# Optimization experiments

Measured on AMD Instinct MI355X. Metric: run time of the kernel, lower is better.

The kernel has to match this reference:

```python
import jax, jax.numpy as jnp
import numpy as np

EPS = 1e-8      # laplace_transform epsilon
RC = 0.5        # residual_coff
L = 2           # num_layers
NU, NB, NI, D = 100000, 30000, 50000, 128
E_UB, E_UI, E_BI = 300000, 500000, 500000


def _l2norm(x):
    # F.normalize(x, p=2, dim=1)
    n = jnp.linalg.norm(x, axis=1, keepdims=True)
    return x / jnp.maximum(n, 1e-12)


def _spmm(rows, cols, vals, feats, n):
    # sparse (COO) matmul: out[r] += vals[e] * feats[cols[e]]
    return jax.ops.segment_sum(vals[:, None] * feats[cols], rows, num_segments=n)


def _sym_norm_graph(u, v, na, nb):
    # bipartite block matrix [[0, B],[B^T, 0]] with D^-1/2 A D^-1/2 normalization
    rows = jnp.concatenate([u, v + na])
    cols = jnp.concatenate([v + na, u])
    deg = jax.ops.segment_sum(jnp.ones(rows.shape[0], jnp.float32), rows,
                              num_segments=na + nb)
    dinv = 1.0 / (jnp.sqrt(deg) + EPS)
    vals = dinv[rows] * dinv[cols]
    return rows, cols, vals


def _one_propagate(rows, cols, vals, afeat, bfeat):
    n = afeat.shape[0] + bfeat.shape[0]
    feats = jnp.concatenate([afeat, bfeat], axis=0)
    ini = _l2norm(feats)
    acc = feats  # all_feats starts with raw feats, summed at the end
    for i in range(L):
        feats = _spmm(rows, cols, vals, feats, n)
        feats = (feats + RC * ini) / (i + 2)
        feats = _l2norm(feats)
        acc = acc + feats
    return acc[:afeat.shape[0]], acc[afeat.shape[0]:]


def setup_inputs() -> dict:
    key = jax.random.key(0)
    ks = jax.random.split(key, 10)
    return {
        "users_feat": jax.random.normal(ks[0], (NU, D), jnp.float32) * 0.1,
        "bundles_feat": jax.random.normal(ks[1], (NB, D), jnp.float32) * 0.1,
        "items_feat": jax.random.normal(ks[2], (NI, D), jnp.float32) * 0.1,
        "bi_vals": jax.random.uniform(ks[3], (E_BI,), jnp.float32),
        "ub_u": jax.random.randint(ks[4], (E_UB,), 0, NU),
        "ub_b": jax.random.randint(ks[5], (E_UB,), 0, NB),
        "ui_u": jax.random.randint(ks[6], (E_UI,), 0, NU),
        "ui_i": jax.random.randint(ks[7], (E_UI,), 0, NI),
        "bi_b": jax.random.randint(ks[8], (E_BI,), 0, NB),
        "bi_i": jax.random.randint(ks[9], (E_BI,), 0, NI),
    }


def reference(users_feat, bundles_feat, items_feat, bi_vals,
              ub_u, ub_b, ui_u, ui_i, bi_b, bi_i):
    nu, nb, ni = users_feat.shape[0], bundles_feat.shape[0], items_feat.shape[0]
    # UB (history) propagation
    r, c, v = _sym_norm_graph(ub_u, ub_b, nu, nb)
    hist_users, hist_bundles = _one_propagate(r, c, v, users_feat, bundles_feat)
    # UI (affinity) propagation
    r, c, v = _sym_norm_graph(ui_u, ui_i, nu, ni)
    aff_users, ui_items = _one_propagate(r, c, v, users_feat, items_feat)
    # BI aggregation: bundles x items sparse graph @ item features
    aff_bundles = _spmm(bi_b, bi_i, bi_vals, ui_items, nb)
    # concat [aff_users, hist_users, aff_bundles, hist_bundles] along rows
    return jnp.concatenate([aff_users, hist_users, aff_bundles, hist_bundles], axis=0)
```

## Files before the change

### kernel.cpp

```cpp
#include <hip/hip_runtime.h>

#define FD   128
#define FDH  64
#define EPSN 1e-8f
#define RCC  0.5f
#define SCAN_TPB 256
#define SCAN_ELEMS 1024

typedef unsigned int uint;
typedef unsigned short u16;
typedef unsigned char u8;
typedef float fx2 __attribute__((ext_vector_type(2)));

__device__ __forceinline__ float wave_sum(float x) {
#pragma unroll
    for (int off = 32; off > 0; off >>= 1) x += __shfl_xor(x, off);
    return x;
}

__device__ __forceinline__ uint packbf2(float a, float b) {
    uint ua = __float_as_uint(a); ua += 0x7fffu + ((ua >> 16) & 1u);
    uint ub = __float_as_uint(b); ub += 0x7fffu + ((ub >> 16) & 1u);
    return (ua >> 16) | (ub & 0xffff0000u);
}
__device__ __forceinline__ float2 unpackbf2(uint v) {
    return make_float2(__uint_as_float(v << 16), __uint_as_float(v & 0xffff0000u));
}
__device__ __forceinline__ u16 packfp8(float a, float b) {
    return (u16)__builtin_amdgcn_cvt_pk_fp8_f32(a, b, 0, false);
}

__global__ void passA(const int* __restrict__ ub_u, const int* __restrict__ ub_b,
                      const int* __restrict__ ui_u, const int* __restrict__ ui_i,
                      const int* __restrict__ bi_b, const int* __restrict__ bi_i,
                      const float* __restrict__ uf, const float* __restrict__ bf,
                      const float* __restrict__ itf,
                      int E_UB, int E_UI, int E_BI, int NU, int NB, int n1, int n2, int NT,
                      int nblk_edges,
                      int* __restrict__ head, int2* __restrict__ pairLL,
                      uint* __restrict__ fini16, float* __restrict__ normf) {
    if ((int)blockIdx.x < nblk_edges) {
        int e = blockIdx.x * blockDim.x + threadIdx.x;
        if (e < E_UB) {
            int a = ub_u[e], b = ub_b[e] + NU;
            int s0 = 2 * e;
            int p0 = atomicExch(&head[a], s0);
            int p1 = atomicExch(&head[b], s0 + 1);
            ((int4*)pairLL)[e] = make_int4(p0, b, p1, a);
        } else if (e < E_UB + E_UI) {
            int f = e - E_UB;
            int a = ui_u[f], bl = ui_i[f] + NU;
            int s0 = 2 * E_UB + 2 * f;
            int p0 = atomicExch(&head[n1 + a], s0);
            int p1 = atomicExch(&head[n1 + bl], s0 + 1);
            ((int4*)pairLL)[E_UB + f] = make_int4(p0, bl, p1, a);
        } else if (e < E_UB + E_UI + E_BI) {
            int g = e - E_UB - E_UI;
            int s = 2 * E_UB + 2 * E_UI + g;
            int p = atomicExch(&head[n1 + n2 + bi_b[g]], s);
            pairLL[s] = make_int2(p, bi_i[g]);
        }
    } else {
        int w = (((int)blockIdx.x - nblk_edges) * blockDim.x + threadIdx.x) >> 6;
        int lane = threadIdx.x & 63;
        if (w >= NT) return;
        const float* src = (w < NU) ? uf + (size_t)w * FD
                         : (w < NU + NB) ? bf + (size_t)(w - NU) * FD
                         : itf + (size_t)(w - NU - NB) * FD;
        float2 x = ((const float2*)src)[lane];
        float ss = wave_sum(x.x * x.x + x.y * x.y);
        float nrm = sqrtf(ss);
        float inv = 1.0f / fmaxf(nrm, 1e-12f);
        fini16[(size_t)w * FDH + lane] = packbf2(x.x * inv, x.y * inv);
        if (lane == 0) normf[w] = nrm;
    }
}

__global__ void passB(const int* __restrict__ head, const int2* __restrict__ pairLL,
                      int NN, int n12, int* __restrict__ deg, float* __restrict__ dinv) {
    int r = blockIdx.x * blockDim.x + threadIdx.x;
    if (r > NN) return;
    if (r == NN) { deg[NN] = 0; return; }
    int c = 0;
    int s = head[r];
    while (s >= 0) { c++; s = pairLL[s].x; }
    deg[r] = c;
    if (r < n12) dinv[r] = 1.0f / (sqrtf((float)c) + EPSN);
}

__global__ void scan_a(const int* __restrict__ in, int* __restrict__ out,
                       int* __restrict__ bsum, int nelem) {
    __shared__ int tsum[SCAN_TPB];
    int tid = threadIdx.x;
    int base = blockIdx.x * SCAN_ELEMS + tid * 4;
    int v0 = (base + 0 < nelem) ? in[base + 0] : 0;
    int v1 = (base + 1 < nelem) ? in[base + 1] : 0;
    int v2 = (base + 2 < nelem) ? in[base + 2] : 0;
    int v3 = (base + 3 < nelem) ? in[base + 3] : 0;
    int s = v0 + v1 + v2 + v3;
    tsum[tid] = s;
    __syncthreads();
    for (int off = 1; off < SCAN_TPB; off <<= 1) {
        int y = (tid >= off) ? tsum[tid - off] : 0;
        __syncthreads();
        tsum[tid] += y;
        __syncthreads();
    }
    int excl = tsum[tid] - s;
    if (tid == SCAN_TPB - 1) bsum[blockIdx.x] = tsum[SCAN_TPB - 1];
    if (base + 0 < nelem) out[base + 0] = excl;
    excl += v0;
    if (base + 1 < nelem) out[base + 1] = excl;
    excl += v1;
    if (base + 2 < nelem) out[base + 2] = excl;
    excl += v2;
    if (base + 3 < nelem) out[base + 3] = excl;
}

__global__ void scan_b(int* __restrict__ bsum, int nb) {
    __shared__ int sm[512];
    int tid = threadIdx.x;
    int v = (tid < nb) ? bsum[tid] : 0;
    sm[tid] = v;
    __syncthreads();
    for (int off = 1; off < 512; off <<= 1) {
        int y = (tid >= off) ? sm[tid - off] : 0;
        __syncthreads();
        sm[tid] += y;
        __syncthreads();
    }
    if (tid < nb) bsum[tid] = sm[tid] - v;
}

__global__ void scan_c(int* __restrict__ out, const int* __restrict__ bsum, int nelem) {
    int base = blockIdx.x * SCAN_ELEMS + threadIdx.x * 4;
    int add = bsum[blockIdx.x];
#pragma unroll
    for (int k = 0; k < 4; ++k)
        if (base + k < nelem) out[base + k] += add;
}

__global__ void passC_conv(const int* __restrict__ head, const int2* __restrict__ pairLL,
                           const int* __restrict__ rowptr, const float* __restrict__ bi_vals,
                           int NN, int n12, int S1,
                           int* __restrict__ cols, int2* __restrict__ bi2,
                           const uint* __restrict__ fini16, const float* __restrict__ normf,
                           const float* __restrict__ dinv,
                           int n1, int NU, int NB, u16* __restrict__ g8, int nblkC) {
    if ((int)blockIdx.x < nblkC) {
        int r = blockIdx.x * blockDim.x + threadIdx.x;
        if (r >= NN) return;
        int pos = rowptr[r];
        int s = head[r];
        if (r < n12) {
            while (s >= 0) { int2 p = pairLL[s]; cols[pos++] = p.y << 7; s = p.x; }
        } else {
            while (s >= 0) {
                int2 p = pairLL[s];
                bi2[pos - S1] = make_int2(p.y << 8, __float_as_int(bi_vals[s - S1]));
                pos++; s = p.x;
            }
        }
    } else {
        int w = (((int)blockIdx.x - nblkC) * blockDim.x + threadIdx.x) >> 6;
        int lane = threadIdx.x & 63;
        if (w >= n12) return;
        int node = (w < n1) ? w : ((w - n1 < NU) ? (w - n1) : (w - n1 + NB));
        float sc = dinv[w] * normf[node];
        float2 f = unpackbf2(fini16[(size_t)node * FDH + lane]);
        g8[(size_t)w * FDH + lane] = packfp8(f.x * sc, f.y * sc);
    }
}

#define ACC8(XU)  {                                                              \
    fx2 _pa = __builtin_amdgcn_cvt_pk_f32_fp8((int)(XU).x, false);               \
    fx2 _pb = __builtin_amdgcn_cvt_pk_f32_fp8((int)(XU).x, true);                \
    fx2 _pc = __builtin_amdgcn_cvt_pk_f32_fp8((int)(XU).y, false);               \
    fx2 _pd = __builtin_amdgcn_cvt_pk_f32_fp8((int)(XU).y, true);                \
    a0 += _pa.x; a1 += _pa.y; a2 += _pb.x; a3 += _pb.y;                          \
    a4 += _pc.x; a5 += _pc.y; a6 += _pd.x; a7 += _pd.y; }

#define GATHER8(TAB)                                                             \
    float a0=0.f,a1=0.f,a2=0.f,a3=0.f,a4=0.f,a5=0.f,a6=0.f,a7=0.f;               \
    {                                                                            \
      int base = lane & 32;                                                      \
      for (int cs = s; cs < e; cs += 32) {                                       \
        int cnt = e - cs; if (cnt > 32) cnt = 32;                                \
        int colv = (l31 < cnt) ? cols[cs + l31] : 0;                             \
        int p = 0;                                                               \
        for (; 2 * p + 8 <= cnt; p += 4) {                                       \
            int o0 = __shfl(colv, base + 2 * p + sub);                           \
            int o1 = __shfl(colv, base + 2 * p + 2 + sub);                       \
            int o2 = __shfl(colv, base + 2 * p + 4 + sub);                       \
            int o3 = __shfl(colv, base + 2 * p + 6 + sub);                       \
            uint2 x0 = *(const uint2*)(TAB + o0);                                \
            uint2 x1 = *(const uint2*)(TAB + o1);                                \
            uint2 x2 = *(const uint2*)(TAB + o2);                                \
            uint2 x3 = *(const uint2*)(TAB + o3);                                \
            ACC8(x0) ACC8(x1) ACC8(x2) ACC8(x3)                                  \
        }                                                                        \
        for (; 2 * p + 2 <= cnt; ++p) {                                          \
            int o = __shfl(colv, base + 2 * p + sub);                            \
            uint2 x = *(const uint2*)(TAB + o);                                  \
            ACC8(x)                                                              \
        }                                                                        \
        if (2 * p < cnt) {                                                       \
            int o = __shfl(colv, base + 2 * p);                                  \
            if (sub == 0) { uint2 x = *(const uint2*)(TAB + o); ACC8(x) }        \
        }                                                                        \
      }                                                                          \
    }                                                                            \
    a0 += __shfl_xor(a0, 16); a1 += __shfl_xor(a1, 16);                          \
    a2 += __shfl_xor(a2, 16); a3 += __shfl_xor(a3, 16);                          \
    a4 += __shfl_xor(a4, 16); a5 += __shfl_xor(a5, 16);                          \
    a6 += __shfl_xor(a6, 16); a7 += __shfl_xor(a7, 16);

__global__ void spmm_L1(const int* __restrict__ rowptr, const int* __restrict__ cols,
                        const float* __restrict__ dinv, const float* __restrict__ normf,
                        const uint* __restrict__ fini16, const u16* __restrict__ g8,
                        uint* __restrict__ facc16, uint* __restrict__ fX8,
                        int n1, int NU, int NB, int n12) {
    int wv = (blockIdx.x * blockDim.x + threadIdx.x) >> 6;
    int lane = threadIdx.x & 63;
    int hw = lane >> 5, l31 = lane & 31, sub = (lane >> 4) & 1, t = lane & 15;
    int r = 2 * wv + hw;
    if (r >= n12) return;
    int s = rowptr[r], e = rowptr[r + 1];
    bool ui = (r >= n1);
    int node = ui ? ((r - n1 < NU) ? (r - n1) : (r - n1 + NB)) : r;
    float dr = dinv[r];
    uint4 iu = ((const uint4*)(fini16 + (size_t)node * FDH))[t];
    float nr = normf[node];
    const u8* tab = (const u8*)g8 + ((size_t)(ui ? n1 : 0) << 7) + (t << 3);
    GATHER8(tab)
    float2 i01 = unpackbf2(iu.x), i23 = unpackbf2(iu.y);
    float2 i45 = unpackbf2(iu.z), i67 = unpackbf2(iu.w);
    float v0 = (dr * a0 + RCC * i01.x) * 0.5f;
    float v1 = (dr * a1 + RCC * i01.y) * 0.5f;
    float v2 = (dr * a2 + RCC * i23.x) * 0.5f;
    float v3 = (dr * a3 + RCC * i23.y) * 0.5f;
    float v4 = (dr * a4 + RCC * i45.x) * 0.5f;
    float v5 = (dr * a5 + RCC * i45.y) * 0.5f;
    float v6 = (dr * a6 + RCC * i67.x) * 0.5f;
    float v7 = (dr * a7 + RCC * i67.y) * 0.5f;
    float sq = v0*v0 + v1*v1 + v2*v2 + v3*v3 + v4*v4 + v5*v5 + v6*v6 + v7*v7;
#pragma unroll
    for (int off = 8; off > 0; off >>= 1) sq += __shfl_xor(sq, off);
    float inv = 1.0f / fmaxf(sqrtf(sq), 1e-12f);
    v0 *= inv; v1 *= inv; v2 *= inv; v3 *= inv;
    v4 *= inv; v5 *= inv; v6 *= inv; v7 *= inv;
    if (sub == 0) {
        uint4 fa;
        fa.x = packbf2(fmaf(i01.x, nr, v0), fmaf(i01.y, nr, v1));
        fa.y = packbf2(fmaf(i23.x, nr, v2), fmaf(i23.y, nr, v3));
        fa.z = packbf2(fmaf(i45.x, nr, v4), fmaf(i45.y, nr, v5));
        fa.w = packbf2(fmaf(i67.x, nr, v6), fmaf(i67.y, nr, v7));
        ((uint4*)(facc16 + (size_t)r * FDH))[t] = fa;
        int xa = __builtin_amdgcn_cvt_pk_fp8_f32(v0 * dr, v1 * dr, 0, false);
        xa = __builtin_amdgcn_cvt_pk_fp8_f32(v2 * dr, v3 * dr, xa, true);
        int xb = __builtin_amdgcn_cvt_pk_fp8_f32(v4 * dr, v5 * dr, 0, false);
        xb = __builtin_amdgcn_cvt_pk_fp8_f32(v6 * dr, v7 * dr, xb, true);
        ((uint2*)(fX8 + (size_t)r * 32))[t] = make_uint2((uint)xa, (uint)xb);
    }
}

__global__ void spmm_L2(const int* __restrict__ rowptr, const int* __restrict__ cols,
                        const float* __restrict__ dinv, const uint* __restrict__ fini16,
                        const uint* __restrict__ facc16, const uint* __restrict__ fX8,
                        uint* __restrict__ items16, float* __restrict__ outp,
                        int n1, int NU, int NB, int n12) {
    int wv = (blockIdx.x * blockDim.x + threadIdx.x) >> 6;
    int lane = threadIdx.x & 63;
    int hw = lane >> 5, l31 = lane & 31, sub = (lane >> 4) & 1, t = lane & 15;
    int r = 2 * wv + hw;
    if (r >= n12) return;
    int s = rowptr[r], e = rowptr[r + 1];
    bool ui = (r >= n1);
    int node = ui ? ((r - n1 < NU) ? (r - n1) : (r - n1 + NB)) : r;
    float dr = dinv[r];
    uint4 iu = ((const uint4*)(fini16 + (size_t)node * FDH))[t];
    uint4 au = ((const uint4*)(facc16 + (size_t)r * FDH))[t];
    const u8* tab = (const u8*)fX8 + ((size_t)(ui ? n1 : 0) << 7) + (t << 3);
    GATHER8(tab)
    float2 i01 = unpackbf2(iu.x), i23 = unpackbf2(iu.y);
    float2 i45 = unpackbf2(iu.z), i67 = unpackbf2(iu.w);
    float v0 = (dr * a0 + RCC * i01.x) * (1.0f / 3.0f);
    float v1 = (dr * a1 + RCC * i01.y) * (1.0f / 3.0f);
    float v2 = (dr * a2 + RCC * i23.x) * (1.0f / 3.0f);
    float v3 = (dr * a3 + RCC * i23.y) * (1.0f / 3.0f);
    float v4 = (dr * a4 + RCC * i45.x) * (1.0f / 3.0f);
    float v5 = (dr * a5 + RCC * i45.y) * (1.0f / 3.0f);
    float v6 = (dr * a6 + RCC * i67.x) * (1.0f / 3.0f);
    float v7 = (dr * a7 + RCC * i67.y) * (1.0f / 3.0f);
    float sq = v0*v0 + v1*v1 + v2*v2 + v3*v3 + v4*v4 + v5*v5 + v6*v6 + v7*v7;
#pragma unroll
    for (int off = 8; off > 0; off >>= 1) sq += __shfl_xor(sq, off);
    float inv = 1.0f / fmaxf(sqrtf(sq), 1e-12f);
    v0 *= inv; v1 *= inv; v2 *= inv; v3 *= inv;
    v4 *= inv; v5 *= inv; v6 *= inv; v7 *= inv;
    float2 a01 = unpackbf2(au.x), a23 = unpackbf2(au.y);
    float2 a45 = unpackbf2(au.z), a67 = unpackbf2(au.w);
    float n0 = a01.x + v0, n1v = a01.y + v1, n2v = a23.x + v2, n3 = a23.y + v3;
    float n4 = a45.x + v4, n5 = a45.y + v5, n6 = a67.x + v6, n7 = a67.y + v7;
    if (sub == 0) {
        if (!ui) {
            size_t dst = (r < NU) ? (size_t)(NU + r) : (size_t)(2 * NU + NB + (r - NU));
            float* orow = outp + dst * FD;
            ((float4*)orow)[2 * t]     = make_float4(n0, n1v, n2v, n3);
            ((float4*)orow)[2 * t + 1] = make_float4(n4, n5, n6, n7);
        } else {
            int l = r - n1;
            if (l < NU) {
                float* orow = outp + (size_t)l * FD;
                ((float4*)orow)[2 * t]     = make_float4(n0, n1v, n2v, n3);
                ((float4*)orow)[2 * t + 1] = make_float4(n4, n5, n6, n7);
            } else {
                uint4 it;
                it.x = packbf2(n0, n1v);
                it.y = packbf2(n2v, n3);
                it.z = packbf2(n4, n5);
                it.w = packbf2(n6, n7);
                ((uint4*)(items16 + (size_t)(l - NU) * FDH))[t] = it;
            }
        }
    }
}

#define FMA8(XU, W) { float2 _f;                                                 \
    _f = unpackbf2((XU).x); a0 = fmaf(W, _f.x, a0); a1 = fmaf(W, _f.y, a1);      \
    _f = unpackbf2((XU).y); a2 = fmaf(W, _f.x, a2); a3 = fmaf(W, _f.y, a3);      \
    _f = unpackbf2((XU).z); a4 = fmaf(W, _f.x, a4); a5 = fmaf(W, _f.y, a5);      \
    _f = unpackbf2((XU).w); a6 = fmaf(W, _f.x, a6); a7 = fmaf(W, _f.y, a7); }

__global__ void bi_gather(const int* __restrict__ rowptr, const int2* __restrict__ bi2,
                          int S1, const uint* __restrict__ items16,
                          float* __restrict__ outb, int nb) {
    int wv = (blockIdx.x * blockDim.x + threadIdx.x) >> 6;
    int lane = threadIdx.x & 63;
    int hw = lane >> 5, l31 = lane & 31, sub = (lane >> 4) & 1, t = lane & 15;
    int r = 2 * wv + hw;
    if (r >= nb) return;
    int s = rowptr[r], e = rowptr[r + 1];
    const u8* tab = (const u8*)items16 + (t << 4);
    float a0=0.f,a1=0.f,a2=0.f,a3=0.f,a4=0.f,a5=0.f,a6=0.f,a7=0.f;
    int base = lane & 32;
    for (int cs = s; cs < e; cs += 32) {
        int cnt = e - cs; if (cnt > 32) cnt = 32;
        int2 cv = (l31 < cnt) ? bi2[cs + l31 - S1] : make_int2(0, 0);
        int p = 0;
        for (; 2 * p + 8 <= cnt; p += 4) {
            int o0 = __shfl(cv.x, base + 2 * p + sub);
            int o1 = __shfl(cv.x, base + 2 * p + 2 + sub);
            int o2 = __shfl(cv.x, base + 2 * p + 4 + sub);
            int o3 = __shfl(cv.x, base + 2 * p + 6 + sub);
            float w0 = __int_as_float(__shfl(cv.y, base + 2 * p + sub));
            float w1 = __int_as_float(__shfl(cv.y, base + 2 * p + 2 + sub));
            float w2 = __int_as_float(__shfl(cv.y, base + 2 * p + 4 + sub));
            float w3 = __int_as_float(__shfl(cv.y, base + 2 * p + 6 + sub));
            uint4 x0 = *(const uint4*)(tab + o0);
            uint4 x1 = *(const uint4*)(tab + o1);
            uint4 x2 = *(const uint4*)(tab + o2);
            uint4 x3 = *(const uint4*)(tab + o3);
            FMA8(x0, w0) FMA8(x1, w1) FMA8(x2, w2) FMA8(x3, w3)
        }
        for (; 2 * p + 2 <= cnt; ++p) {
            int o = __shfl(cv.x, base + 2 * p + sub);
            float wt = __int_as_float(__shfl(cv.y, base + 2 * p + sub));
            uint4 x = *(const uint4*)(tab + o);
            FMA8(x, wt)
        }
        if (2 * p < cnt) {
            int o = __shfl(cv.x, base + 2 * p);
            float wt = __int_as_float(__shfl(cv.y, base + 2 * p));
            if (sub == 0) { uint4 x = *(const uint4*)(tab + o); FMA8(x, wt) }
        }
    }
    a0 += __shfl_xor(a0, 16); a1 += __shfl_xor(a1, 16);
    a2 += __shfl_xor(a2, 16); a3 += __shfl_xor(a3, 16);
    a4 += __shfl_xor(a4, 16); a5 += __shfl_xor(a5, 16);
    a6 += __shfl_xor(a6, 16); a7 += __shfl_xor(a7, 16);
    if (sub == 0) {
        float* orow = outb + (size_t)r * FD;
        ((float4*)orow)[2 * t]     = make_float4(a0, a1, a2, a3);
        ((float4*)orow)[2 * t + 1] = make_float4(a4, a5, a6, a7);
    }
}

extern "C" void kernel_launch(void* const* d_in, const int* in_sizes, int n_in,
                              void* d_out, int out_size, void* d_ws, size_t ws_size,
                              hipStream_t stream) {
    const float* users   = (const float*)d_in[0];
    const float* bundles = (const float*)d_in[1];
    const float* items   = (const float*)d_in[2];
    const float* bi_vals = (const float*)d_in[3];
    const int* ub_u = (const int*)d_in[4];
    const int* ub_b = (const int*)d_in[5];
    const int* ui_u = (const int*)d_in[6];
    const int* ui_i = (const int*)d_in[7];
    const int* bi_b = (const int*)d_in[8];
    const int* bi_i = (const int*)d_in[9];

    const int NU = in_sizes[0] / FD;
    const int NB = in_sizes[1] / FD;
    const int NI = in_sizes[2] / FD;
    const int E_BI = in_sizes[3];
    const int E_UB = in_sizes[4];
    const int E_UI = in_sizes[6];
    float* out = (float*)d_out;

    const int n1 = NU + NB, n2 = NU + NI;
    const int n12 = n1 + n2;
    const int NT = NU + NB + NI;
    const int NN = n12 + NB;
    const int S1 = 2 * E_UB + 2 * E_UI;
    const int TOT = S1 + E_BI;
    const int ETOT = E_UB + E_UI + E_BI;

    uint* fini16   = (uint*)d_ws;
    uint* facc16   = fini16 + (size_t)NT * FDH;
    uint* items16  = facc16 + (size_t)n12 * FDH;
    u16* g8        = (u16*)(items16 + (size_t)NI * FDH);
    uint* fX8      = (uint*)(g8 + (size_t)n12 * FDH);
    float* normf   = (float*)(fX8 + (size_t)n12 * 32);
    float* dinv    = normf + NT;
    int* deg       = (int*)(dinv + n12);
    int* rowptr    = deg + (NN + 1);
    int* head      = rowptr + (NN + 1);
    int* bsum      = head + NN;
    int* cols      = bsum + 512;
    int2* bi2      = (int2*)((((size_t)(cols + S1)) + 15) & ~(size_t)15);
    int2* pairLL   = (int2*)((((size_t)(bi2 + E_BI)) + 15) & ~(size_t)15);

    dim3 blk(256);
    auto rows_grid  = [](int n) { return dim3((unsigned)((n + 3) / 4)); };
    auto rows2_grid = [](int n) { return dim3((unsigned)((n + 7) / 8)); };
    auto thr_grid   = [](int n) { return dim3((unsigned)((n + 255) / 256)); };

    hipMemsetAsync(head, 0xFF, (size_t)NN * 4, stream);
    int nblk_edges = (ETOT + 255) / 256;
    int nblk_prep  = (NT + 3) / 4;
    passA<<<dim3((unsigned)(nblk_edges + nblk_prep)), blk, 0, stream>>>(
        ub_u, ub_b, ui_u, ui_i, bi_b, bi_i, users, bundles, items,
        E_UB, E_UI, E_BI, NU, NB, n1, n2, NT, nblk_edges,
        head, pairLL, fini16, normf);
    passB<<<thr_grid(NN + 1), blk, 0, stream>>>(head, pairLL, NN, n12, deg, dinv);
    {
        int nelem = NN + 1;
        int nblk = (nelem + SCAN_ELEMS - 1) / SCAN_ELEMS;
        scan_a<<<dim3((unsigned)nblk), dim3(SCAN_TPB), 0, stream>>>(deg, rowptr, bsum, nelem);
        scan_b<<<dim3(1), dim3(512), 0, stream>>>(bsum, nblk);
        scan_c<<<dim3((unsigned)nblk), dim3(SCAN_TPB), 0, stream>>>(rowptr, bsum, nelem);
    }
    {
        int nblkC = (NN + 255) / 256;
        int nblkG = (n12 + 3) / 4;
        passC_conv<<<dim3((unsigned)(nblkC + nblkG)), blk, 0, stream>>>(
            head, pairLL, rowptr, bi_vals, NN, n12, S1, cols, bi2,
            fini16, normf, dinv, n1, NU, NB, g8, nblkC);
    }

    spmm_L1<<<rows2_grid(n12), blk, 0, stream>>>(rowptr, cols, dinv, normf,
                                                 fini16, g8, facc16, fX8, n1, NU, NB, n12);
    spmm_L2<<<rows2_grid(n12), blk, 0, stream>>>(rowptr, cols, dinv, fini16,
                                                 facc16, fX8, items16, out, n1, NU, NB, n12);
    bi_gather<<<rows2_grid(NB), blk, 0, stream>>>(rowptr + n12, bi2, S1, items16,
        out + (size_t)2 * NU * FD, NB);
}
```

Measured before the change: 601.8 us.

## Quantize layer-1 propagated features to FP4 with per-row scale for layer-2 gather

```diff
diff --git a/kernel.cpp b/kernel.cpp
--- a/kernel.cpp
+++ b/kernel.cpp
@@ -11,6 +11,18 @@
 typedef unsigned short u16;
 typedef unsigned char u8;
 typedef float fx2 __attribute__((ext_vector_type(2)));
+typedef int iv4 __attribute__((ext_vector_type(4)));
+typedef int iv2 __attribute__((ext_vector_type(2)));
+
+#if __has_builtin(__builtin_amdgcn_cvt_scalef32_pk_f32_fp4) && __has_builtin(__builtin_amdgcn_cvt_scalef32_pk_fp4_f32)
+#define USE_FP4 1
+#define COLSHIFT 6
+#define L1SHIFT 1
+#else
+#define USE_FP4 0
+#define COLSHIFT 7
+#define L1SHIFT 0
+#endif
 
 __device__ __forceinline__ float wave_sum(float x) {
 #pragma unroll
@@ -46,19 +58,22 @@
             int s0 = 2 * e;
             int p0 = atomicExch(&head[a], s0);
             int p1 = atomicExch(&head[b], s0 + 1);
-            ((int4*)pairLL)[e] = make_int4(p0, b, p1, a);
+            iv4 rec = {p0, b, p1, a};
+            __builtin_nontemporal_store(rec, (iv4*)pairLL + e);
         } else if (e < E_UB + E_UI) {
             int f = e - E_UB;
             int a = ui_u[f], bl = ui_i[f] + NU;
             int s0 = 2 * E_UB + 2 * f;
             int p0 = atomicExch(&head[n1 + a], s0);
             int p1 = atomicExch(&head[n1 + bl], s0 + 1);
-            ((int4*)pairLL)[E_UB + f] = make_int4(p0, bl, p1, a);
+            iv4 rec = {p0, bl, p1, a};
+            __builtin_nontemporal_store(rec, (iv4*)pairLL + (E_UB + f));
         } else if (e < E_UB + E_UI + E_BI) {
             int g = e - E_UB - E_UI;
             int s = 2 * E_UB + 2 * E_UI + g;
             int p = atomicExch(&head[n1 + n2 + bi_b[g]], s);
-            pairLL[s] = make_int2(p, bi_i[g]);
+            iv2 rec = {p, bi_i[g]};
+            __builtin_nontemporal_store(rec, (iv2*)pairLL + s);
         }
     } else {
         int w = (((int)blockIdx.x - nblk_edges) * blockDim.x + threadIdx.x) >> 6;
@@ -71,7 +86,8 @@
         float ss = wave_sum(x.x * x.x + x.y * x.y);
         float nrm = sqrtf(ss);
         float inv = 1.0f / fmaxf(nrm, 1e-12f);
-        fini16[(size_t)w * FDH + lane] = packbf2(x.x * inv, x.y * inv);
+        __builtin_nontemporal_store(packbf2(x.x * inv, x.y * inv),
+                                    &fini16[(size_t)w * FDH + lane]);
         if (lane == 0) normf[w] = nrm;
     }
 }
@@ -153,7 +169,7 @@
         int pos = rowptr[r];
         int s = head[r];
         if (r < n12) {
-            while (s >= 0) { int2 p = pairLL[s]; cols[pos++] = p.y << 7; s = p.x; }
+            while (s >= 0) { int2 p = pairLL[s]; cols[pos++] = p.y << COLSHIFT; s = p.x; }
         } else {
             while (s >= 0) {
                 int2 p = pairLL[s];
@@ -180,7 +196,7 @@
     a0 += _pa.x; a1 += _pa.y; a2 += _pb.x; a3 += _pb.y;                          \
     a4 += _pc.x; a5 += _pc.y; a6 += _pd.x; a7 += _pd.y; }
 
-#define GATHER8(TAB)                                                             \
+#define GATHER8(TAB, SH)                                                         \
     float a0=0.f,a1=0.f,a2=0.f,a3=0.f,a4=0.f,a5=0.f,a6=0.f,a7=0.f;               \
     {                                                                            \
       int base = lane & 32;                                                      \
@@ -189,10 +205,10 @@
         int colv = (l31 < cnt) ? cols[cs + l31] : 0;                             \
         int p = 0;                                                               \
         for (; 2 * p + 8 <= cnt; p += 4) {                                       \
-            int o0 = __shfl(colv, base + 2 * p + sub);                           \
-            int o1 = __shfl(colv, base + 2 * p + 2 + sub);                       \
-            int o2 = __shfl(colv, base + 2 * p + 4 + sub);                       \
-            int o3 = __shfl(colv, base + 2 * p + 6 + sub);                       \
+            int o0 = __shfl(colv, base + 2 * p + sub) << (SH);                   \
+            int o1 = __shfl(colv, base + 2 * p + 2 + sub) << (SH);               \
+            int o2 = __shfl(colv, base + 2 * p + 4 + sub) << (SH);               \
+            int o3 = __shfl(colv, base + 2 * p + 6 + sub) << (SH);               \
             uint2 x0 = *(const uint2*)(TAB + o0);                                \
             uint2 x1 = *(const uint2*)(TAB + o1);                                \
             uint2 x2 = *(const uint2*)(TAB + o2);                                \
@@ -200,12 +216,12 @@
             ACC8(x0) ACC8(x1) ACC8(x2) ACC8(x3)                                  \
         }                                                                        \
         for (; 2 * p + 2 <= cnt; ++p) {                                          \
-            int o = __shfl(colv, base + 2 * p + sub);                            \
+            int o = __shfl(colv, base + 2 * p + sub) << (SH);                    \
             uint2 x = *(const uint2*)(TAB + o);                                  \
             ACC8(x)                                                              \
         }                                                                        \
         if (2 * p < cnt) {                                                       \
-            int o = __shfl(colv, base + 2 * p);                                  \
+            int o = __shfl(colv, base + 2 * p) << (SH);                          \
             if (sub == 0) { uint2 x = *(const uint2*)(TAB + o); ACC8(x) }        \
         }                                                                        \
       }                                                                          \
@@ -215,10 +231,66 @@
     a4 += __shfl_xor(a4, 16); a5 += __shfl_xor(a5, 16);                          \
     a6 += __shfl_xor(a6, 16); a7 += __shfl_xor(a7, 16);
 
+#if USE_FP4
+#define ACC4(XU, SV)  {                                                          \
+    fx2 _f;                                                                      \
+    _f = __builtin_amdgcn_cvt_scalef32_pk_f32_fp4((XU), 1.0f, 0);                \
+    a0 = fmaf(SV, _f.x, a0); a1 = fmaf(SV, _f.y, a1);                            \
+    _f = __builtin_amdgcn_cvt_scalef32_pk_f32_fp4((XU), 1.0f, 1);                \
+    a2 = fmaf(SV, _f.x, a2); a3 = fmaf(SV, _f.y, a3);                            \
+    _f = __builtin_amdgcn_cvt_scalef32_pk_f32_fp4((XU), 1.0f, 2);                \
+    a4 = fmaf(SV, _f.x, a4); a5 = fmaf(SV, _f.y, a5);                            \
+    _f = __builtin_amdgcn_cvt_scalef32_pk_f32_fp4((XU), 1.0f, 3);                \
+    a6 = fmaf(SV, _f.x, a6); a7 = fmaf(SV, _f.y, a7); }
+
+#define GATHER4(TAB, FSC)                                                        \
+    float a0=0.f,a1=0.f,a2=0.f,a3=0.f,a4=0.f,a5=0.f,a6=0.f,a7=0.f;               \
+    {                                                                            \
+      int base = lane & 32;                                                      \
+      for (int cs = s; cs < e; cs += 32) {                                       \
+        int cnt = e - cs; if (cnt > 32) cnt = 32;                                \
+        int colv = (l31 < cnt) ? cols[cs + l31] : 0;                             \
+        float sclv = (FSC)[colv >> 6];                                           \
+        int p = 0;                                                               \
+        for (; 2 * p + 8 <= cnt; p += 4) {                                       \
+            int o0 = __shfl(colv, base + 2 * p + sub);                           \
+            int o1 = __shfl(colv, base + 2 * p + 2 + sub);                       \
+            int o2 = __shfl(colv, base + 2 * p + 4 + sub);                       \
+            int o3 = __shfl(colv, base + 2 * p + 6 + sub);                       \
+            float s0v = __shfl(sclv, base + 2 * p + sub);                        \
+            float s1v = __shfl(sclv, base + 2 * p + 2 + sub);                    \
+            float s2v = __shfl(sclv, base + 2 * p + 4 + sub);                    \
+            float s3v = __shfl(sclv, base + 2 * p + 6 + sub);                    \
+            uint x0 = *(const uint*)(TAB + o0);                                  \
+            uint x1 = *(const uint*)(TAB + o1);                                  \
+            uint x2 = *(const uint*)(TAB + o2);                                  \
+            uint x3 = *(const uint*)(TAB + o3);                                  \
+            ACC4(x0, s0v) ACC4(x1, s1v) ACC4(x2, s2v) ACC4(x3, s3v)              \
+        }                                                                        \
+        for (; 2 * p + 2 <= cnt; ++p) {                                          \
+            int o = __shfl(colv, base + 2 * p + sub);                            \
+            float sv = __shfl(sclv, base + 2 * p + sub);                         \
+            uint x = *(const uint*)(TAB + o);                                    \
+            ACC4(x, sv)                                                          \
+        }                                                                        \
+        if (2 * p < cnt) {                                                       \
+            int o = __shfl(colv, base + 2 * p);                                  \
+            float sv = __shfl(sclv, base + 2 * p);                               \
+            if (sub == 0) { uint x = *(const uint*)(TAB + o); ACC4(x, sv) }      \
+        }                                                                        \
+      }                                                                          \
+    }                                                                            \
+    a0 += __shfl_xor(a0, 16); a1 += __shfl_xor(a1, 16);                          \
+    a2 += __shfl_xor(a2, 16); a3 += __shfl_xor(a3, 16);                          \
+    a4 += __shfl_xor(a4, 16); a5 += __shfl_xor(a5, 16);                          \
+    a6 += __shfl_xor(a6, 16); a7 += __shfl_xor(a7, 16);
+#endif
+
 __global__ void spmm_L1(const int* __restrict__ rowptr, const int* __restrict__ cols,
                         const float* __restrict__ dinv, const float* __restrict__ normf,
                         const uint* __restrict__ fini16, const u16* __restrict__ g8,
-                        uint* __restrict__ facc16, uint* __restrict__ fX8,
+                        uint* __restrict__ facc16, uint* __restrict__ fX,
+                        float* __restrict__ fscale,
                         int n1, int NU, int NB, int n12) {
     int wv = (blockIdx.x * blockDim.x + threadIdx.x) >> 6;
     int lane = threadIdx.x & 63;
@@ -232,7 +304,7 @@
     uint4 iu = ((const uint4*)(fini16 + (size_t)node * FDH))[t];
     float nr = normf[node];
     const u8* tab = (const u8*)g8 + ((size_t)(ui ? n1 : 0) << 7) + (t << 3);
-    GATHER8(tab)
+    GATHER8(tab, L1SHIFT)
     float2 i01 = unpackbf2(iu.x), i23 = unpackbf2(iu.y);
     float2 i45 = unpackbf2(iu.z), i67 = unpackbf2(iu.w);
     float v0 = (dr * a0 + RCC * i01.x) * 0.5f;
@@ -256,17 +328,37 @@
         fa.z = packbf2(fmaf(i45.x, nr, v4), fmaf(i45.y, nr, v5));
         fa.w = packbf2(fmaf(i67.x, nr, v6), fmaf(i67.y, nr, v7));
         ((uint4*)(facc16 + (size_t)r * FDH))[t] = fa;
+#if USE_FP4
+        float q0 = v0 * dr, q1 = v1 * dr, q2 = v2 * dr, q3 = v3 * dr;
+        float q4 = v4 * dr, q5 = v5 * dr, q6 = v6 * dr, q7 = v7 * dr;
+        float m = fmaxf(fmaxf(fmaxf(fabsf(q0), fabsf(q1)), fmaxf(fabsf(q2), fabsf(q3))),
+                        fmaxf(fmaxf(fabsf(q4), fabsf(q5)), fmaxf(fabsf(q6), fabsf(q7))));
+        m = fmaxf(m, __shfl_xor(m, 1));
+        m = fmaxf(m, __shfl_xor(m, 2));
+        m = fmaxf(m, __shfl_xor(m, 4));
+        m = fmaxf(m, __shfl_xor(m, 8));
+        float sc = fmaxf(m, 1e-30f) * (1.0f / 6.0f);
+        float isc = 1.0f / sc;
+        if (t == 0) fscale[r] = sc;
+        int xa = __builtin_amdgcn_cvt_scalef32_pk_fp4_f32(0,  q0 * isc, q1 * isc, 1.0f, 0);
+        xa = __builtin_amdgcn_cvt_scalef32_pk_fp4_f32(xa, q2 * isc, q3 * isc, 1.0f, 1);
+        xa = __builtin_amdgcn_cvt_scalef32_pk_fp4_f32(xa, q4 * isc, q5 * isc, 1.0f, 2);
+        xa = __builtin_amdgcn_cvt_scalef32_pk_fp4_f32(xa, q6 * isc, q7 * isc, 1.0f, 3);
+        fX[(size_t)r * 16 + t] = (uint)xa;
+#else
         int xa = __builtin_amdgcn_cvt_pk_fp8_f32(v0 * dr, v1 * dr, 0, false);
         xa = __builtin_amdgcn_cvt_pk_fp8_f32(v2 * dr, v3 * dr, xa, true);
         int xb = __builtin_amdgcn_cvt_pk_fp8_f32(v4 * dr, v5 * dr, 0, false);
         xb = __builtin_amdgcn_cvt_pk_fp8_f32(v6 * dr, v7 * dr, xb, true);
-        ((uint2*)(fX8 + (size_t)r * 32))[t] = make_uint2((uint)xa, (uint)xb);
+        ((uint2*)(fX + (size_t)r * 32))[t] = make_uint2((uint)xa, (uint)xb);
+#endif
     }
 }
 
 __global__ void spmm_L2(const int* __restrict__ rowptr, const int* __restrict__ cols,
                         const float* __restrict__ dinv, const uint* __restrict__ fini16,
-                        const uint* __restrict__ facc16, const uint* __restrict__ fX8,
+                        const uint* __restrict__ facc16, const uint* __restrict__ fX,
+                        const float* __restrict__ fscale,
                         uint* __restrict__ items16, float* __restrict__ outp,
                         int n1, int NU, int NB, int n12) {
     int wv = (blockIdx.x * blockDim.x + threadIdx.x) >> 6;
@@ -280,8 +372,14 @@
     float dr = dinv[r];
     uint4 iu = ((const uint4*)(fini16 + (size_t)node * FDH))[t];
     uint4 au = ((const uint4*)(facc16 + (size_t)r * FDH))[t];
-    const u8* tab = (const u8*)fX8 + ((size_t)(ui ? n1 : 0) << 7) + (t << 3);
-    GATHER8(tab)
+#if USE_FP4
+    const u8* tab = (const u8*)fX + ((size_t)(ui ? n1 : 0) << 6) + (t << 2);
+    const float* fsc = fscale + (ui ? n1 : 0);
+    GATHER4(tab, fsc)
+#else
+    const u8* tab = (const u8*)fX + ((size_t)(ui ? n1 : 0) << 7) + (t << 3);
+    GATHER8(tab, 0)
+#endif
     float2 i01 = unpackbf2(iu.x), i23 = unpackbf2(iu.y);
     float2 i45 = unpackbf2(iu.z), i67 = unpackbf2(iu.w);
     float v0 = (dr * a0 + RCC * i01.x) * (1.0f / 3.0f);
@@ -420,8 +518,9 @@
     uint* facc16   = fini16 + (size_t)NT * FDH;
     uint* items16  = facc16 + (size_t)n12 * FDH;
     u16* g8        = (u16*)(items16 + (size_t)NI * FDH);
-    uint* fX8      = (uint*)(g8 + (size_t)n12 * FDH);
-    float* normf   = (float*)(fX8 + (size_t)n12 * 32);
+    uint* fX       = (uint*)(g8 + (size_t)n12 * FDH);
+    float* fscale  = (float*)(fX + (size_t)n12 * 32);
+    float* normf   = fscale + n12;
     float* dinv    = normf + NT;
     int* deg       = (int*)(dinv + n12);
     int* rowptr    = deg + (NN + 1);
@@ -432,7 +531,6 @@
     int2* pairLL   = (int2*)((((size_t)(bi2 + E_BI)) + 15) & ~(size_t)15);
 
     dim3 blk(256);
-    auto rows_grid  = [](int n) { return dim3((unsigned)((n + 3) / 4)); };
     auto rows2_grid = [](int n) { return dim3((unsigned)((n + 7) / 8)); };
     auto thr_grid   = [](int n) { return dim3((unsigned)((n + 255) / 256)); };
 
@@ -460,9 +558,11 @@
     }
 
     spmm_L1<<<rows2_grid(n12), blk, 0, stream>>>(rowptr, cols, dinv, normf,
-                                                 fini16, g8, facc16, fX8, n1, NU, NB, n12);
+                                                 fini16, g8, facc16, fX, fscale,
+                                                 n1, NU, NB, n12);
     spmm_L2<<<rows2_grid(n12), blk, 0, stream>>>(rowptr, cols, dinv, fini16,
-                                                 facc16, fX8, items16, out, n1, NU, NB, n12);
+                                                 facc16, fX, fscale, items16, out,
+                                                 n1, NU, NB, n12);
     bi_gather<<<rows2_grid(NB), blk, 0, stream>>>(rowptr + n12, bi2, S1, items16,
         out + (size_t)2 * NU * FD, NB);
 }
```

Result: slower. 624.2 us (+3.7%).
